# Optimization experiments

Measured on AMD Instinct MI355X. Metric: run time of the kernel, lower is better.

The kernel has to match this reference:

```python
import jax, jax.numpy as jnp
import numpy as np

PUSH_MARGIN = 1.0
NUM_LABELS = 65  # label ids 0..64; 0 = background (skipped)
EPS = 1e-12


def _safe_norm(d, axis):
    # L2 norm with grad-safe sqrt at 0 (matches ||.||_2 value everywhere relevant)
    sq = jnp.sum(d * d, axis=axis)
    return jnp.sqrt(jnp.maximum(sq, EPS))


def setup_inputs() -> dict:
    key = jax.random.key(0)
    k1, k2, k3 = jax.random.split(key, 3)
    B, N, C, H, W = 16, 16384, 128, 512, 512
    abs_embedding = jax.random.normal(k1, (B, N, C), dtype=jnp.float32)
    coordinates = jax.random.randint(k2, (B, N, 2), 0, H, dtype=jnp.int32)
    y = jax.random.randint(k3, (B, H, W), 0, NUM_LABELS, dtype=jnp.int32)
    return {"abs_embedding": abs_embedding, "coordinates": coordinates, "y": y}


def reference(abs_embedding, coordinates, y):
    def per_image(emb, coords, yb):
        # emb: [N,C], coords: [N,2], yb: [H,W]
        labels = yb[coords[:, 0], coords[:, 1]]                       # [N]
        ones = jnp.ones(labels.shape, emb.dtype)
        counts = jax.ops.segment_sum(ones, labels, num_segments=NUM_LABELS)   # [L]
        sums = jax.ops.segment_sum(emb, labels, num_segments=NUM_LABELS)      # [L,C]
        centroids = sums / jnp.maximum(counts, 1.0)[:, None]                   # [L,C]
        # pull: per-instance mean distance of samples to their centroid, summed over fg instances
        d = _safe_norm(emb - centroids[labels], axis=-1)              # [N]
        dist_sum = jax.ops.segment_sum(d, labels, num_segments=NUM_LABELS)
        fg_counts = counts[1:]
        present = fg_counts > 0
        pull = jnp.sum(jnp.where(present, dist_sum[1:] / jnp.maximum(fg_counts, 1.0), 0.0))
        # push: mean over strict-upper-tri pairs of relu(margin - ||c_i - c_j||)
        c = centroids[1:]                                             # [K,C]
        dm = _safe_norm(c[:, None, :] - c[None, :, :], axis=-1)        # [K,K]
        push_vals = jax.nn.relu(PUSH_MARGIN - dm)
        K = c.shape[0]
        tri = jnp.triu(jnp.ones((K, K), bool), k=1)
        pair_mask = tri & present[:, None] & present[None, :]
        npairs = jnp.maximum(jnp.sum(pair_mask.astype(emb.dtype)), 1.0)
        push = jnp.sum(jnp.where(pair_mask, push_vals, 0.0)) / npairs
        return pull + push

    per_b = jax.vmap(per_image)(abs_embedding, coordinates, y)        # [B]
    return jnp.sum(per_b)
```

## Files before the change

kernel.cpp:

```cpp
#include <hip/hip_runtime.h>

#define B_ 16
#define N_ 16384
#define C_ 128
#define H_ 512
#define W_ 512
#define L_ 65
#define FG 64

#define OFF_SUMS 0
#define OFF_CNT  (B_*L_*C_)
#define OFF_DIST (OFF_CNT + B_*L_)
#define OFF_LAB  (OFF_DIST + B_*L_)
#define OFF_BCNT (OFF_LAB + B_*N_)

#define APB 512
#define DPB 256
#define PREP_BLOCKS (B_*N_/256)

__global__ __launch_bounds__(256) void k_prep(const int2* __restrict__ coords,
                                              const int* __restrict__ y,
                                              float* __restrict__ ws,
                                              float* __restrict__ out) {
    __shared__ int s_cnt[L_];
    const int gid = blockIdx.x * 256 + threadIdx.x;
    if (threadIdx.x < L_) s_cnt[threadIdx.x] = 0;
    if (gid < OFF_CNT) ws[gid] = 0.f;
    if (gid < B_ * L_) ws[OFF_DIST + gid] = 0.f;
    if (gid == 0) out[0] = 0.f;
    __syncthreads();
    const int b = gid >> 14;
    int2 rc = coords[gid];
    int lab = y[(b << 18) + (rc.x << 9) + rc.y];
    ((int*)(ws + OFF_LAB))[gid] = lab;
    atomicAdd(&s_cnt[lab], 1);
    __syncthreads();
    if (threadIdx.x < L_)
        ((int*)(ws + OFF_BCNT))[blockIdx.x * L_ + threadIdx.x] = s_cnt[threadIdx.x];
}

__global__ __launch_bounds__(256) void k_accum(const float* __restrict__ emb,
                                               float* __restrict__ ws) {
    __shared__ float4 s_sum4[2 * L_ * 32];
    __shared__ int s_lab[APB];
    const int b = blockIdx.x >> 5;
    const int base = (blockIdx.x & 31) * APB;
    const int wave = threadIdx.x >> 6;
    const int lane = threadIdx.x & 63;
    const int half = lane >> 5, j = lane & 31;

    const float4 zero4 = {0.f, 0.f, 0.f, 0.f};
    for (int i = threadIdx.x; i < 2 * L_ * 32; i += 256) s_sum4[i] = zero4;
    const int* labg = (const int*)(ws + OFF_LAB) + b * N_ + base;
    for (int i = threadIdx.x; i < APB; i += 256) s_lab[i] = labg[i];
    __syncthreads();

    const float4* embp = (const float4*)(emb + (size_t)b * N_ * C_
                                         + (size_t)(base + wave * (APB / 4)) * C_) + j;
    const int* labp = s_lab + wave * (APB / 4);
    float4* copy = s_sum4 + half * (L_ * 32) + j;

#define LOADB(e, lb, s) do {                                   \
        _Pragma("unroll")                                      \
        for (int u = 0; u < 8; ++u) {                          \
            int p = 2 * ((s) * 8 + u) + half;                  \
            e[u]  = embp[(size_t)p * 32];   \
            lb[u] = labp[p];                \
        } } while (0)

#define RMWB(e, lb) do {                                       \
        _Pragma("unroll")                                      \
        for (int u = 0; u < 8; ++u) {                          \
            float4 v = copy[lb[u] * 32];                       \
            v.x += e[u].x; v.y += e[u].y;                      \
            v.z += e[u].z; v.w += e[u].w;                      \
            copy[lb[u] * 32] = v;                              \
        } } while (0)

    float4 eA[8], eB[8]; int lbA[8], lbB[8];
    LOADB(eA, lbA, 0);
    LOADB(eB, lbB, 1);
    RMWB(eA, lbA);
    LOADB(eA, lbA, 2);
    RMWB(eB, lbB);
    LOADB(eB, lbB, 3);
    RMWB(eA, lbA);
    LOADB(eA, lbA, 4);
    RMWB(eB, lbB);
    LOADB(eB, lbB, 5);
    RMWB(eA, lbA);
    LOADB(eA, lbA, 6);
    RMWB(eB, lbB);
    LOADB(eB, lbB, 7);
    RMWB(eA, lbA);
    RMWB(eB, lbB);
#undef LOADB
#undef RMWB

    __syncthreads();
    float* gs = ws + OFF_SUMS + b * L_ * C_;
    const float* ss = (const float*)s_sum4;
    for (int i = threadIdx.x; i < L_ * C_; i += 256)
        unsafeAtomicAdd(&gs[i], ss[i] + ss[L_ * C_ + i]);
}

__global__ __launch_bounds__(256) void k_cent(float* __restrict__ ws) {
    __shared__ float s_inv[L_];
    const int b = blockIdx.x;
    const int t = threadIdx.x;
    if (t < L_) {
        const int* bc = (const int*)(ws + OFF_BCNT);
        int c = 0;
        #pragma unroll 8
        for (int k = 0; k < PREP_BLOCKS / B_; ++k)
            c += bc[(b * (PREP_BLOCKS / B_) + k) * L_ + t];
        ((int*)(ws + OFF_CNT))[b * L_ + t] = c;
        s_inv[t] = 1.f / fmaxf((float)c, 1.f);
    }
    __syncthreads();
    float* gs = ws + OFF_SUMS + b * L_ * C_;
    for (int i = t; i < L_ * C_; i += 256) gs[i] *= s_inv[i >> 7];
}

__global__ __launch_bounds__(256) void k_dist(const float* __restrict__ emb,
                                              float* __restrict__ ws) {
    __shared__ __align__(16) float4 s_cent4[L_ * 33];
    __shared__ float s_dist[L_];
    const int b = blockIdx.x >> 6;
    const int base = (blockIdx.x & 63) * DPB;

    const float* gcent = ws + OFF_SUMS + b * L_ * C_;
    for (int i = threadIdx.x; i < L_ * 32; i += 256) {
        int l = i >> 5, q = i & 31;
        s_cent4[l * 33 + q] = ((const float4*)gcent)[l * 32 + q];
    }
    if (threadIdx.x < L_) s_dist[threadIdx.x] = 0.f;
    __syncthreads();

    const int p = base + threadIdx.x;
    const int lb = ((const int*)(ws + OFF_LAB))[b * N_ + p];
    const float4* ep = (const float4*)(emb + (size_t)b * N_ * C_) + (size_t)p * 32;
    const float4* cp = s_cent4 + lb * 33;
    float acc = 0.f;
    #pragma unroll 8
    for (int q = 0; q < 32; ++q) {
        float4 e = ep[q], c = cp[q];
        float dx = e.x - c.x, dy = e.y - c.y;
        float dz = e.z - c.z, dw = e.w - c.w;
        acc += dx * dx + dy * dy + dz * dz + dw * dw;
    }
    unsafeAtomicAdd(&s_dist[lb], sqrtf(fmaxf(acc, 1e-12f)));
    __syncthreads();
    if (threadIdx.x < L_) {
        float d = s_dist[threadIdx.x];
        if (d != 0.f) unsafeAtomicAdd(ws + OFF_DIST + b * L_ + threadIdx.x, d);
    }
}

#define CSTRIDE 132

__global__ __launch_bounds__(256) void k_final(float* __restrict__ ws, float* __restrict__ out) {
    __shared__ __align__(16) float s_cc[FG * CSTRIDE];
    __shared__ float s_present[FG];
    __shared__ float s_red[3];
    const int b = blockIdx.x;
    const int t = threadIdx.x;

    const float* gcent = ws + OFF_SUMS + b * L_ * C_;
    for (int i = t; i < FG * C_; i += 256) {
        int l = i >> 7, ch = i & 127;
        s_cc[l * CSTRIDE + ch] = gcent[(l + 1) * C_ + ch];
    }
    if (t < 3) s_red[t] = 0.f;
    if (t < FG) {
        int cnt = ((const int*)(ws + OFF_CNT))[b * L_ + 1 + t];
        s_present[t] = (cnt > 0) ? 1.f : 0.f;
        float pl = (cnt > 0) ? ws[OFF_DIST + b * L_ + 1 + t] / (float)cnt : 0.f;
        #pragma unroll
        for (int off = 32; off; off >>= 1) pl += __shfl_xor(pl, off);
        if (t == 0) s_red[0] = pl;
    }
    __syncthreads();

    const int wave = t >> 6, lane = t & 63;
    const int ti = lane >> 3, tj = lane & 7;
    float psum = 0.f, pnp = 0.f;
    for (int tt = wave; tt < 36; tt += 4) {
        int a = 0, c = tt;
        while (c >= 8 - a) { c -= 8 - a; ++a; }
        c += a;
        int i = a * 8 + ti, jx = c * 8 + tj;
        float acc = 0.f;
        #pragma unroll
        for (int ch = 0; ch < C_; ch += 4) {
            float4 xi = *(const float4*)&s_cc[i * CSTRIDE + ch];
            float4 xj = *(const float4*)&s_cc[jx * CSTRIDE + ch];
            float dx = xi.x - xj.x, dy = xi.y - xj.y;
            float dz = xi.z - xj.z, dw = xi.w - xj.w;
            acc += dx * dx + dy * dy + dz * dz + dw * dw;
        }
        float dm = sqrtf(fmaxf(acc, 1e-12f));
        float pv = fmaxf(1.f - dm, 0.f);
        bool valid = (i < jx) && (s_present[i] > 0.f) && (s_present[jx] > 0.f);
        if (valid) { psum += pv; pnp += 1.f; }
    }
    #pragma unroll
    for (int off = 32; off; off >>= 1) {
        psum += __shfl_xor(psum, off);
        pnp  += __shfl_xor(pnp,  off);
    }
    if (lane == 0) { unsafeAtomicAdd(&s_red[1], psum); unsafeAtomicAdd(&s_red[2], pnp); }
    __syncthreads();
    if (t == 0) {
        float loss = s_red[0] + s_red[1] / fmaxf(s_red[2], 1.f);
        unsafeAtomicAdd(out, loss);
    }
}

extern "C" void kernel_launch(void* const* d_in, const int* in_sizes, int n_in,
                              void* d_out, int out_size, void* d_ws, size_t ws_size,
                              hipStream_t stream) {
    const float* emb   = (const float*)d_in[0];
    const int2* coords = (const int2*)d_in[1];
    const int*  y      = (const int*)d_in[2];
    float* out = (float*)d_out;
    float* ws  = (float*)d_ws;

    k_prep<<<PREP_BLOCKS, 256, 0, stream>>>(coords, y, ws, out);
    k_accum<<<B_ * (N_ / APB), 256, 0, stream>>>(emb, ws);
    k_cent<<<B_, 256, 0, stream>>>(ws);
    k_dist<<<B_ * (N_ / DPB), 256, 0, stream>>>(emb, ws);
    k_final<<<B_, 256, 0, stream>>>(ws, out);
}
```

Measured before the change: 256.6 us.

## Replace global atomic centroid accumulation with per-block partials reduced in k_cent

k_accum now writes its per-block label sums to a partials buffer instead of atomically adding them into the global sums. k_cent is widened to 8 blocks per image, and those blocks reduce the 32 partials per image and apply the count normalization. This is meant to remove contended global float atomics, and it no longer needs the sums zeroed in k_prep. The trade-off is extra workspace traffic for writing and reading the partial buffers, plus an extra reduction pass.

```diff
diff --git a/kernel.cpp b/kernel.cpp
--- a/kernel.cpp
+++ b/kernel.cpp
@@ -13,6 +13,7 @@
 #define OFF_DIST (OFF_CNT + B_*L_)
 #define OFF_LAB  (OFF_DIST + B_*L_)
 #define OFF_BCNT (OFF_LAB + B_*N_)
+#define OFF_PART (OFF_BCNT + 1024*L_)
 
 #define APB 512
 #define DPB 256
@@ -25,7 +26,6 @@
     __shared__ int s_cnt[L_];
     const int gid = blockIdx.x * 256 + threadIdx.x;
     if (threadIdx.x < L_) s_cnt[threadIdx.x] = 0;
-    if (gid < OFF_CNT) ws[gid] = 0.f;
     if (gid < B_ * L_) ws[OFF_DIST + gid] = 0.f;
     if (gid == 0) out[0] = 0.f;
     __syncthreads();
@@ -98,28 +98,41 @@
 #undef RMWB
 
     __syncthreads();
-    float* gs = ws + OFF_SUMS + b * L_ * C_;
-    const float* ss = (const float*)s_sum4;
-    for (int i = threadIdx.x; i < L_ * C_; i += 256)
-        unsafeAtomicAdd(&gs[i], ss[i] + ss[L_ * C_ + i]);
+    float4* gp4 = (float4*)(ws + OFF_PART) + (size_t)blockIdx.x * (L_ * 32);
+    for (int i = threadIdx.x; i < L_ * 32; i += 256) {
+        float4 a = s_sum4[i], c = s_sum4[L_ * 32 + i];
+        a.x += c.x; a.y += c.y; a.z += c.z; a.w += c.w;
+        gp4[i] = a;
+    }
 }
 
 __global__ __launch_bounds__(256) void k_cent(float* __restrict__ ws) {
     __shared__ float s_inv[L_];
-    const int b = blockIdx.x;
+    const int b = blockIdx.x >> 3, c = blockIdx.x & 7;
     const int t = threadIdx.x;
     if (t < L_) {
         const int* bc = (const int*)(ws + OFF_BCNT);
-        int c = 0;
+        int cnt = 0;
         #pragma unroll 8
         for (int k = 0; k < PREP_BLOCKS / B_; ++k)
-            c += bc[(b * (PREP_BLOCKS / B_) + k) * L_ + t];
-        ((int*)(ws + OFF_CNT))[b * L_ + t] = c;
-        s_inv[t] = 1.f / fmaxf((float)c, 1.f);
-    }
-    __syncthreads();
-    float* gs = ws + OFF_SUMS + b * L_ * C_;
-    for (int i = t; i < L_ * C_; i += 256) gs[i] *= s_inv[i >> 7];
+            cnt += bc[(b * (PREP_BLOCKS / B_) + k) * L_ + t];
+        if (c == 0) ((int*)(ws + OFF_CNT))[b * L_ + t] = cnt;
+        s_inv[t] = 1.f / fmaxf((float)cnt, 1.f);
+    }
+    __syncthreads();
+    const float4* part = (const float4*)(ws + OFF_PART) + (size_t)b * 32 * (L_ * 32);
+    float4* gs = (float4*)(ws + OFF_SUMS) + (size_t)b * (L_ * 32);
+    for (int i4 = c * 260 + t; i4 < (c + 1) * 260 && i4 < L_ * 32; i4 += 256) {
+        float4 s = {0.f, 0.f, 0.f, 0.f};
+        #pragma unroll 8
+        for (int s0 = 0; s0 < 32; ++s0) {
+            float4 p = part[(size_t)s0 * (L_ * 32) + i4];
+            s.x += p.x; s.y += p.y; s.z += p.z; s.w += p.w;
+        }
+        float inv = s_inv[(i4 * 4) >> 7];
+        s.x *= inv; s.y *= inv; s.z *= inv; s.w *= inv;
+        gs[i4] = s;
+    }
 }
 
 __global__ __launch_bounds__(256) void k_dist(const float* __restrict__ emb,
@@ -228,7 +241,7 @@
 
     k_prep<<<PREP_BLOCKS, 256, 0, stream>>>(coords, y, ws, out);
     k_accum<<<B_ * (N_ / APB), 256, 0, stream>>>(emb, ws);
-    k_cent<<<B_, 256, 0, stream>>>(ws);
+    k_cent<<<B_ * 8, 256, 0, stream>>>(ws);
     k_dist<<<B_ * (N_ / DPB), 256, 0, stream>>>(emb, ws);
     k_final<<<B_, 256, 0, stream>>>(ws, out);
 }
```

Result: no change. 253.0 us (-1.4%).
